# Kernel tuning notes

Measured on AMD Instinct MI355X. Metric: run time of the kernel, lower is better.

## Reference

```python
import math
import jax, jax.numpy as jnp
import numpy as np

R, C, D, ORDER = 2048, 2048, 64, 3
O = ORDER + 1  # var_size


def setup_inputs() -> dict:
    key = jax.random.key(0)
    k1, k2, k3, k4, k5, k6 = jax.random.split(key, 6)
    return {
        "events": jax.random.randint(k1, (R, C), 0, 2, dtype=jnp.int32),
        "col_times": jax.random.uniform(k2, (C,), dtype=jnp.float32),
        "z_rows": jax.random.normal(k3, (O, R, D), dtype=jnp.float32),
        "z_cols": jax.random.normal(k4, (C, D), dtype=jnp.float32),
        "gamma_rows": jax.random.uniform(k5, (R,), dtype=jnp.float32),
        "gamma_cols": jax.random.uniform(k6, (C,), dtype=jnp.float32),
    }


def reference(events, col_times, z_rows, z_cols, gamma_rows, gamma_cols):
    o = z_rows.shape[0]
    facts = np.array([math.factorial(i) for i in range(o)], dtype=np.float32)
    # Taylor time-basis: coeffs[o, c] = t_c^o / o!   (replaces nested Python loops)
    coeffs = jnp.stack([col_times ** i for i in range(o)]) / facts[:, None]  # (O, C)
    # row positions at each column's time: (R, C, D)
    pos = jnp.einsum('ord,oc->rcd', z_rows, coeffs)
    diff = pos - z_cols[None, :, :]                        # (R, C, D)
    dist = jnp.sqrt(jnp.sum(diff * diff, axis=-1))         # (R, C) pairwise L2
    logit = gamma_rows[:, None] + gamma_cols[None, :] - dist
    # log p where p = 1 - E - (1-2E)*sigmoid(logit):
    #   E==1 -> log sigmoid(logit); E==0 -> log sigmoid(-logit)
    sign = jnp.where(events == 1, 1.0, -1.0).astype(logit.dtype)
    log_lik = jnp.sum(jax.nn.log_sigmoid(sign * logit))
    return -log_lik
```

## Files before the change

kernel.cpp:

```cpp
#include <hip/hip_runtime.h>
#include <hip/hip_bf16.h>
#include <math.h>

#define R_DIM 2048
#define C_DIM 2048
#define D_DIM 64
#define KSTRIDE 168

typedef __attribute__((ext_vector_type(8))) short short8;
typedef __attribute__((ext_vector_type(4))) float floatx4;

__device__ __forceinline__ ushort f2bf(float f) {
  unsigned u = __float_as_uint(f);
  return (ushort)((u + 0x7FFFu + ((u >> 16) & 1u)) >> 16);
}
__device__ __forceinline__ ushort4 pack4(float4 v) {
  ushort4 r;
  r.x = f2bf(v.x); r.y = f2bf(v.y); r.z = f2bf(v.z); r.w = f2bf(v.w);
  return r;
}
__device__ __forceinline__ float4 scale4(float s, float4 v) {
  float4 r;
  r.x = s * v.x; r.y = s * v.y; r.z = s * v.z; r.w = s * v.w;
  return r;
}
__device__ __forceinline__ float dot4(float4 a, float4 b) {
  return fmaf(a.x, b.x, fmaf(a.y, b.y, fmaf(a.z, b.z, a.w * b.w)));
}

__launch_bounds__(256, 3)
__global__ void fused_kernel(const int* __restrict__ events,
                             const float* __restrict__ col_times,
                             const float* __restrict__ z_rows,
                             const float* __restrict__ z_cols,
                             const float* __restrict__ gamma_rows,
                             const float* __restrict__ gamma_cols,
                             unsigned* __restrict__ cnt,
                             float* __restrict__ parts,
                             float* __restrict__ out) {
  __shared__ __align__(16) ushort As[64 * KSTRIDE];
  __shared__ __align__(16) ushort Bs[64 * KSTRIDE];
  __shared__ float nzc_s[64];
  __shared__ float red[4];
  __shared__ float flag;

  const int t = threadIdx.x;
  const int widx = t >> 6, lane = t & 63;
  const int m0 = blockIdx.y * 64, c0 = blockIdx.x * 64;
  const int wm = widx & 1, wn = widx >> 1;
  const int lm = lane & 15, kg = lane >> 4;

  const int rr = t >> 2;
  const int ch = t & 3;
  const int d0 = ch * 16;

  float4 av[4][4];
#pragma unroll
  for (int o = 0; o < 4; ++o)
#pragma unroll
    for (int i = 0; i < 4; ++i)
      av[o][i] = *(const float4*)&z_rows[(size_t)(o * R_DIM + m0 + rr) * D_DIM + d0 + i * 4];
  float4 bv[4];
#pragma unroll
  for (int i = 0; i < 4; ++i)
    bv[i] = *(const float4*)&z_cols[(size_t)(c0 + rr) * D_DIM + d0 + i * 4];
  const float tt = col_times[c0 + rr];
  float cf[4];
  cf[0] = 1.0f; cf[1] = tt; cf[2] = tt * tt * 0.5f; cf[3] = cf[2] * tt * (1.0f / 3.0f);

#pragma unroll
  for (int o = 0; o < 2; ++o) {
    const float s = -2.0f * cf[o];
#pragma unroll
    for (int i = 0; i < 4; ++i) {
      *(ushort4*)&As[rr * KSTRIDE + o * 64 + d0 + i * 4] = pack4(av[o][i]);
      *(ushort4*)&Bs[rr * KSTRIDE + o * 64 + d0 + i * 4] = pack4(scale4(s, bv[i]));
    }
  }
  float q = dot4(bv[0], bv[0]) + dot4(bv[1], bv[1]) + dot4(bv[2], bv[2]) + dot4(bv[3], bv[3]);
  q += __shfl_xor(q, 1); q += __shfl_xor(q, 2);
  if (ch == 0) nzc_s[rr] = q;

  __syncthreads();

  floatx4 acc[2][2];
#pragma unroll
  for (int i = 0; i < 2; ++i)
#pragma unroll
    for (int j = 0; j < 2; ++j) acc[i][j] = (floatx4){0.f, 0.f, 0.f, 0.f};

#pragma unroll
  for (int kt = 0; kt < 128; kt += 32) {
    short8 a[2], b[2];
#pragma unroll
    for (int mt = 0; mt < 2; ++mt)
      a[mt] = *(const short8*)&As[(wm * 32 + mt * 16 + lm) * KSTRIDE + kt + kg * 8];
#pragma unroll
    for (int nt = 0; nt < 2; ++nt)
      b[nt] = *(const short8*)&Bs[(wn * 32 + nt * 16 + lm) * KSTRIDE + kt + kg * 8];
#pragma unroll
    for (int mt = 0; mt < 2; ++mt)
#pragma unroll
      for (int nt = 0; nt < 2; ++nt)
        acc[mt][nt] = __builtin_amdgcn_mfma_f32_16x16x32_bf16(a[mt], b[nt], acc[mt][nt], 0, 0, 0);
  }

  __syncthreads();

#pragma unroll
  for (int o = 2; o < 4; ++o) {
    const float s = -2.0f * cf[o];
#pragma unroll
    for (int i = 0; i < 4; ++i) {
      *(ushort4*)&As[rr * KSTRIDE + (o - 2) * 64 + d0 + i * 4] = pack4(av[o][i]);
      *(ushort4*)&Bs[rr * KSTRIDE + (o - 2) * 64 + d0 + i * 4] = pack4(scale4(s, bv[i]));
    }
  }
  float g[10];
#pragma unroll
  for (int p = 0; p < 10; ++p) g[p] = 0.0f;
#pragma unroll
  for (int i = 0; i < 4; ++i) {
    const float4 a0 = av[0][i], a1 = av[1][i], a2 = av[2][i], a3 = av[3][i];
    g[0] += dot4(a0, a0); g[1] += dot4(a0, a1); g[2] += dot4(a0, a2);
    g[3] += dot4(a0, a3); g[4] += dot4(a1, a1); g[5] += dot4(a1, a2);
    g[6] += dot4(a1, a3); g[7] += dot4(a2, a2); g[8] += dot4(a2, a3);
    g[9] += dot4(a3, a3);
  }
#pragma unroll
  for (int p = 0; p < 10; ++p) {
    g[p] += __shfl_xor(g[p], 1);
    g[p] += __shfl_xor(g[p], 2);
  }
  if (ch == 0) {
    ushort* ea = &As[rr * KSTRIDE + 128];
    ea[0] = f2bf(g[0]); ea[1] = f2bf(g[1]); ea[2] = f2bf(g[2]); ea[3] = f2bf(g[3]);
    ea[4] = f2bf(g[1]); ea[5] = f2bf(g[4]); ea[6] = f2bf(g[5]); ea[7] = f2bf(g[6]);
    ea[8] = f2bf(g[2]); ea[9] = f2bf(g[5]); ea[10] = f2bf(g[7]); ea[11] = f2bf(g[8]);
    ea[12] = f2bf(g[3]); ea[13] = f2bf(g[6]); ea[14] = f2bf(g[8]); ea[15] = f2bf(g[9]);
#pragma unroll
    for (int z = 16; z < 32; ++z) ea[z] = 0;
    ushort* eb = &Bs[rr * KSTRIDE + 128];
#pragma unroll
    for (int i = 0; i < 16; ++i) eb[i] = f2bf(cf[i >> 2] * cf[i & 3]);
#pragma unroll
    for (int z = 16; z < 32; ++z) eb[z] = 0;
  }
  __syncthreads();

#pragma unroll
  for (int kt = 0; kt < 160; kt += 32) {
    short8 a[2], b[2];
#pragma unroll
    for (int mt = 0; mt < 2; ++mt)
      a[mt] = *(const short8*)&As[(wm * 32 + mt * 16 + lm) * KSTRIDE + kt + kg * 8];
#pragma unroll
    for (int nt = 0; nt < 2; ++nt)
      b[nt] = *(const short8*)&Bs[(wn * 32 + nt * 16 + lm) * KSTRIDE + kt + kg * 8];
#pragma unroll
    for (int mt = 0; mt < 2; ++mt)
#pragma unroll
      for (int nt = 0; nt < 2; ++nt)
        acc[mt][nt] = __builtin_amdgcn_mfma_f32_16x16x32_bf16(a[mt], b[nt], acc[mt][nt], 0, 0, 0);
  }

  float gc[2], nz[2];
  int cidx[2];
#pragma unroll
  for (int nt = 0; nt < 2; ++nt) {
    const int c = c0 + wn * 32 + nt * 16 + lm;
    cidx[nt] = c;
    gc[nt] = gamma_cols[c];
    nz[nt] = nzc_s[c - c0];
  }
  float lsum = 0.0f;
#pragma unroll
  for (int mt = 0; mt < 2; ++mt) {
    const int rbase = m0 + wm * 32 + mt * 16 + kg * 4;
#pragma unroll
    for (int j = 0; j < 4; ++j) {
      const int r = rbase + j;
      const float gr = gamma_rows[r];
#pragma unroll
      for (int nt = 0; nt < 2; ++nt) {
        const int ev = events[(size_t)r * C_DIM + cidx[nt]];
        const float d2 = acc[mt][nt][j] + nz[nt];
        const float dist = sqrtf(fmaxf(d2, 0.0f));
        const float logit = gr + gc[nt] - dist;
        const float x = ev ? -logit : logit;
        lsum += fmaxf(x, 0.0f) + __logf(1.0f + __expf(-fabsf(x)));
      }
    }
  }
#pragma unroll
  for (int off = 32; off > 0; off >>= 1) lsum += __shfl_down(lsum, off);
  if (lane == 0) red[widx] = lsum;
  __syncthreads();

  const int bid = blockIdx.y * gridDim.x + blockIdx.x;
  if (t == 0) {
    const float bs = red[0] + red[1] + red[2] + red[3];
    atomicExch(&parts[bid], bs);
    __threadfence();
    const unsigned old = atomicAdd(cnt, 1u);
    flag = (old == 1023u) ? 1.0f : 0.0f;
  }
  __syncthreads();
  if (flag != 0.0f) {
    __threadfence();
    float s = 0.0f;
    for (int i = t; i < 1024; i += 256) s += atomicAdd(&parts[i], 0.0f);
#pragma unroll
    for (int off = 32; off > 0; off >>= 1) s += __shfl_down(s, off);
    if (lane == 0) red[widx] = s;
    __syncthreads();
    if (t == 0) out[0] = red[0] + red[1] + red[2] + red[3];
  }
}

extern "C" void kernel_launch(void* const* d_in, const int* in_sizes, int n_in,
                              void* d_out, int out_size, void* d_ws, size_t ws_size,
                              hipStream_t stream) {
  const int* events = (const int*)d_in[0];
  const float* col_times = (const float*)d_in[1];
  const float* z_rows = (const float*)d_in[2];
  const float* z_cols = (const float*)d_in[3];
  const float* gamma_rows = (const float*)d_in[4];
  const float* gamma_cols = (const float*)d_in[5];

  unsigned* cnt = (unsigned*)d_ws;
  float* parts = (float*)d_ws + 16;
  hipMemsetAsync(d_ws, 0, 4, stream);

  dim3 grid(C_DIM / 64, R_DIM / 64);
  fused_kernel<<<grid, 256, 0, stream>>>(events, col_times, z_rows, z_cols,
                                         gamma_rows, gamma_cols, cnt, parts,
                                         (float*)d_out);
}
```

Baseline: 109.6 us.

## Prefetch events tile with vector loads into LDS bytes before MFMA

Events for the 64x64 tile are now loaded early with coalesced int4 loads, overlapping their latency with the MFMA work. They are then packed to bytes in shared memory and read back in the MFMA output layout, replacing the old scattered 4-byte global reads in the epilogue. The log-sigmoid is also rewritten as softplus(logit) - e*logit, which removes the sign select. This adds registers held across the GEMM, an extra LDS buffer, and a barrier, which may lower occupancy.

```diff
diff --git a/kernel.cpp b/kernel.cpp
--- a/kernel.cpp
+++ b/kernel.cpp
@@ -40,6 +40,7 @@
                              float* __restrict__ out) {
   __shared__ __align__(16) ushort As[64 * KSTRIDE];
   __shared__ __align__(16) ushort Bs[64 * KSTRIDE];
+  __shared__ __align__(16) unsigned char Evb[64 * 64];
   __shared__ float nzc_s[64];
   __shared__ float red[4];
   __shared__ float flag;
@@ -65,6 +66,14 @@
   for (int i = 0; i < 4; ++i)
     bv[i] = *(const float4*)&z_cols[(size_t)(c0 + rr) * D_DIM + d0 + i * 4];
   const float tt = col_times[c0 + rr];
+
+  const int erow = t >> 4;
+  const int ecol = (t & 15) * 4;
+  int4 evr[4];
+#pragma unroll
+  for (int i = 0; i < 4; ++i)
+    evr[i] = *(const int4*)&events[(size_t)(m0 + i * 16 + erow) * C_DIM + c0 + ecol];
+
   float cf[4];
   cf[0] = 1.0f; cf[1] = tt; cf[2] = tt * tt * 0.5f; cf[3] = cf[2] * tt * (1.0f / 3.0f);
 
@@ -164,31 +173,38 @@
         acc[mt][nt] = __builtin_amdgcn_mfma_f32_16x16x32_bf16(a[mt], b[nt], acc[mt][nt], 0, 0, 0);
   }
 
+#pragma unroll
+  for (int i = 0; i < 4; ++i) {
+    uchar4 pk;
+    pk.x = (unsigned char)evr[i].x; pk.y = (unsigned char)evr[i].y;
+    pk.z = (unsigned char)evr[i].z; pk.w = (unsigned char)evr[i].w;
+    *(uchar4*)&Evb[(i * 16 + erow) * 64 + ecol] = pk;
+  }
+  __syncthreads();
+
   float gc[2], nz[2];
-  int cidx[2];
+  int cl[2];
 #pragma unroll
   for (int nt = 0; nt < 2; ++nt) {
     const int c = c0 + wn * 32 + nt * 16 + lm;
-    cidx[nt] = c;
+    cl[nt] = wn * 32 + nt * 16 + lm;
     gc[nt] = gamma_cols[c];
-    nz[nt] = nzc_s[c - c0];
+    nz[nt] = nzc_s[cl[nt]];
   }
   float lsum = 0.0f;
 #pragma unroll
   for (int mt = 0; mt < 2; ++mt) {
-    const int rbase = m0 + wm * 32 + mt * 16 + kg * 4;
+    const int rl = wm * 32 + mt * 16 + kg * 4;
 #pragma unroll
     for (int j = 0; j < 4; ++j) {
-      const int r = rbase + j;
-      const float gr = gamma_rows[r];
+      const float gr = gamma_rows[m0 + rl + j];
 #pragma unroll
       for (int nt = 0; nt < 2; ++nt) {
-        const int ev = events[(size_t)r * C_DIM + cidx[nt]];
+        const float evf = (float)Evb[(rl + j) * 64 + cl[nt]];
         const float d2 = acc[mt][nt][j] + nz[nt];
         const float dist = sqrtf(fmaxf(d2, 0.0f));
         const float logit = gr + gc[nt] - dist;
-        const float x = ev ? -logit : logit;
-        lsum += fmaxf(x, 0.0f) + __logf(1.0f + __expf(-fabsf(x)));
+        lsum += fmaxf(logit, 0.0f) + __logf(1.0f + __expf(-fabsf(logit))) - evf * logit;
       }
     }
   }
```

New measurement: 107.0 us. -2.4%, faster.
